# Optimization experiments

Hardware: AMD Instinct MI355X
Metric: run time of the kernel (lower is better)

The kernel has to match this reference:

```python
import jax, jax.numpy as jnp
import numpy as np

N = 30000
E = 480000
D_IN = 128
EPS = 1e-5
NEG_SLOPE = 0.2
# (in_dim, out_channels, heads) per GATConv layer; concat=True everywhere (PyG default)
CFG = [(D_IN, 100, 5), (500, 50, 5), (250, 32, 4), (128, 8, 4), (32, 1, 1)]
BN_DIMS = (500, 250, 128)


def setup_inputs() -> dict:
    key = jax.random.key(0)
    ks = iter(jax.random.split(key, 80))
    inp = {
        "x": jax.random.normal(next(ks), (N, D_IN), jnp.float32),
        "edge_index": jax.random.randint(next(ks), (2, E), 0, N),
        "edge_weight": jax.random.uniform(next(ks), (E, 1), jnp.float32),
    }
    for l, (cin, cout, h) in enumerate(CFG, 1):
        s = 1.0 / np.sqrt(cin)
        inp[f"W{l}"] = jax.random.normal(next(ks), (cin, h * cout), jnp.float32) * s
        inp[f"a_s{l}"] = jax.random.normal(next(ks), (1, h, cout), jnp.float32) * 0.1
        inp[f"a_d{l}"] = jax.random.normal(next(ks), (1, h, cout), jnp.float32) * 0.1
        inp[f"We{l}"] = jax.random.normal(next(ks), (1, h * cout), jnp.float32)
        inp[f"a_e{l}"] = jax.random.normal(next(ks), (1, h, cout), jnp.float32) * 0.1
        inp[f"b{l}"] = jnp.zeros((h * cout,), jnp.float32)
    for l, d in zip((1, 2, 3), BN_DIMS):
        inp[f"g{l}"] = jnp.ones((d,), jnp.float32)
        inp[f"beta{l}"] = jnp.zeros((d,), jnp.float32)
    return inp


def _gat(x, src, dst, ea, W, a_s, a_d, We, a_e, b, heads, cout):
    """PyG GATConv with edge_dim attention (concat=True)."""
    n = x.shape[0]
    h = (x @ W).reshape(n, heads, cout)            # [N,H,C]
    e = (ea @ We).reshape(-1, heads, cout)         # [E,H,C]
    al_src = (h * a_s).sum(-1)                     # [N,H]
    al_dst = (h * a_d).sum(-1)                     # [N,H]
    logit = jax.nn.leaky_relu(al_src[src] + al_dst[dst] + (e * a_e).sum(-1), NEG_SLOPE)
    m = jax.ops.segment_max(logit, dst, num_segments=n)
    m = jnp.where(jnp.isfinite(m), m, 0.0)
    ex = jnp.exp(logit - m[dst])                   # [E,H]
    den = jax.ops.segment_sum(ex, dst, num_segments=n)
    alpha = ex / jnp.maximum(den[dst], 1e-16)      # segment softmax over in-edges of dst
    out = jax.ops.segment_sum(h[src] * alpha[..., None], dst, num_segments=n)
    return out.reshape(n, heads * cout) + b


def _bn(x, g, b):
    mu = x.mean(0)
    var = x.var(0)  # biased, as torch uses for normalization
    return (x - mu) * jax.lax.rsqrt(var + EPS) * g + b


def reference(x, edge_index, edge_weight,
              W1, a_s1, a_d1, We1, a_e1, b1,
              W2, a_s2, a_d2, We2, a_e2, b2,
              W3, a_s3, a_d3, We3, a_e3, b3,
              W4, a_s4, a_d4, We4, a_e4, b4,
              W5, a_s5, a_d5, We5, a_e5, b5,
              g1, beta1, g2, beta2, g3, beta3):
    # add self loops (PyG default) with edge_attr fill_value='mean'
    loop = jnp.arange(N)
    src = jnp.concatenate([edge_index[0], loop])
    dst = jnp.concatenate([edge_index[1], loop])
    ea = jnp.concatenate([edge_weight, jnp.full((N, 1), edge_weight.mean(), edge_weight.dtype)], axis=0)

    h = _gat(x, src, dst, ea, W1, a_s1, a_d1, We1, a_e1, b1, 5, 100)
    h = jax.nn.relu(_bn(h, g1, beta1))
    h = _gat(h, src, dst, ea, W2, a_s2, a_d2, We2, a_e2, b2, 5, 50)
    h = jax.nn.relu(_bn(h, g2, beta2))
    h = _gat(h, src, dst, ea, W3, a_s3, a_d3, We3, a_e3, b3, 4, 32)
    h = jax.nn.relu(_bn(h, g3, beta3))
    h = _gat(h, src, dst, ea, W4, a_s4, a_d4, We4, a_e4, b4, 4, 8)
    h = jax.nn.relu(h)
    h = _gat(h, src, dst, ea, W5, a_s5, a_d5, We5, a_e5, b5, 1, 1)
    return h
```

## Files before the change

### kernel.cpp

```cpp
#include <hip/hip_runtime.h>
#include <hip/hip_bf16.h>
#include <math.h>

#define NN 30000
#define EE 480000
#define ET (EE + NN)
#define NEG_SLOPE 0.2f
#define BN_EPS 1e-5f

struct LayerCfg { int cin, C, H; };
static const LayerCfg g_cfg[5] = {
    {128, 100, 5}, {500, 50, 5}, {250, 32, 4}, {128, 8, 4}, {32, 1, 1}
};

typedef short short8 __attribute__((ext_vector_type(8)));
typedef float f32x4 __attribute__((ext_vector_type(4)));

__device__ __forceinline__ unsigned short f2bf(float f) {
    unsigned int u = __builtin_bit_cast(unsigned int, f);
    u = (u + 0x7FFFu + ((u >> 16) & 1u)) >> 16;
    return (unsigned short)u;
}
__device__ __forceinline__ float bf2f(unsigned short h) {
    unsigned int u = ((unsigned int)h) << 16;
    return __builtin_bit_cast(float, u);
}


__global__ void ewsum_kernel(const float* __restrict__ ew, float* __restrict__ out, int E) {
    __shared__ float sdata[256];
    int tid = threadIdx.x;
    float s = 0.f;
    for (int i = blockIdx.x * blockDim.x + tid; i < E; i += gridDim.x * blockDim.x)
        s += ew[i];
    sdata[tid] = s;
    __syncthreads();
    for (int off = 128; off > 0; off >>= 1) {
        if (tid < off) sdata[tid] += sdata[tid + off];
        __syncthreads();
    }
    if (tid == 0) atomicAdd(out, sdata[0]);
}

__global__ void build_edges_kernel(const int* __restrict__ ei, const float* __restrict__ ew,
                                   const float* __restrict__ sum,
                                   int* __restrict__ srcv, int* __restrict__ dstv,
                                   float* __restrict__ ea, int* __restrict__ cnt) {
    int e = blockIdx.x * blockDim.x + threadIdx.x;
    if (e >= ET) return;
    int d;
    if (e < EE) {
        srcv[e] = ei[e];
        d = ei[EE + e];
        dstv[e] = d;
        ea[e]   = ew[e];
    } else {
        int n = e - EE;
        srcv[e] = n;
        d = n;
        dstv[e] = n;
        ea[e]   = sum[0] * (1.0f / (float)EE);
    }
    atomicAdd(&cnt[d], 1);
}

__global__ void scan_kernel(const int* __restrict__ cnt, int* __restrict__ off,
                            int* __restrict__ wptr) {
    __shared__ int lsum[1024];
    __shared__ int loff[1024];
    const int T = 1024;
    int t = threadIdx.x;
    int chunk = (NN + T - 1) / T;
    int base = t * chunk;
    int end = min(NN, base + chunk);
    int s = 0;
    for (int i = base; i < end; i++) s += cnt[i];
    lsum[t] = s;
    __syncthreads();
    if (t == 0) {
        int run = 0;
        for (int i = 0; i < T; i++) { loff[i] = run; run += lsum[i]; }
    }
    __syncthreads();
    int run = loff[t];
    for (int i = base; i < end; i++) {
        off[i] = run;
        wptr[i] = run;
        run += cnt[i];
    }
    if (t == 0) off[NN] = ET;
}

__global__ void fill_kernel(const int* __restrict__ dstv, const int* __restrict__ srcv,
                            const float* __restrict__ ea,
                            int* __restrict__ wptr, int* __restrict__ csr_src,
                            float* __restrict__ csr_ea) {
    int e = blockIdx.x * blockDim.x + threadIdx.x;
    if (e >= ET) return;
    int p = atomicAdd(&wptr[dstv[e]], 1);
    csr_src[p] = srcv[e];
    csr_ea[p]  = ea[e];
}


struct PrepArgs {
    const float* W[5];
    const float* We[5];
    const float* ae[5];
    unsigned short* bh[5];
    unsigned short* bl[5];
    float* wedot;
    int K[5], N[5], Kp[5], Np[5], C[5], H[5];
};

__global__ void wedot_all_kernel(PrepArgs a) {
    int tid = threadIdx.x;
    int l = tid >> 3, hd = tid & 7;
    if (l < 5 && hd < a.H[l]) {
        int C = a.C[l];
        const float* We = a.We[l] + hd * C;
        const float* ae = a.ae[l] + hd * C;
        float s = 0.f;
        for (int c = 0; c < C; c++) s += We[c] * ae[c];
        a.wedot[l * 8 + hd] = s;
    }
}

__global__ void transpose_all_kernel(PrepArgs a) {
    int l = blockIdx.z;
    int Kp = a.Kp[l], Np = a.Np[l], K = a.K[l], N = a.N[l];
    int kb = blockIdx.x * 32, nb = blockIdx.y * 32;
    if (kb >= Kp || nb >= Np) return;
    const float* B = a.W[l];
    unsigned short* Bth = a.bh[l];
    unsigned short* Btl = a.bl[l];
    __shared__ float tile[32][33];
    int tx = threadIdx.x, ty = threadIdx.y;
#pragma unroll
    for (int i = 0; i < 4; i++) {
        int k = kb + ty + i * 8, n = nb + tx;
        tile[ty + i * 8][tx] = (k < K && n < N) ? B[(size_t)k * N + n] : 0.f;
    }
    __syncthreads();
#pragma unroll
    for (int i = 0; i < 4; i++) {
        int n = nb + ty + i * 8, k = kb + tx;
        if (n < Np && k < Kp) {
            float v = tile[tx][ty + i * 8];
            unsigned short hi = f2bf(v);
            unsigned short lo = f2bf(v - bf2f(hi));
            size_t idx = (size_t)n * Kp + k;
            Bth[idx] = hi;
            Btl[idx] = lo;
        }
    }
}

#define GBM 128
#define GBNT 128
#define GBK 32
#define ASTR 36
__global__ __launch_bounds__(256) void gemm_split_kernel(const float* __restrict__ A,
                                                         const unsigned short* __restrict__ Bt_hi,
                                                         const unsigned short* __restrict__ Bt_lo,
                                                         float* __restrict__ Cm,
                                                         unsigned short* __restrict__ Ch16,
                                                         int M, int Kp, int Nc,
                                                         const float* __restrict__ colsum,
                                                         const float* __restrict__ colsumsq,
                                                         const float* __restrict__ g,
                                                         const float* __restrict__ beta,
                                                         int D) {
    __shared__ short AsH[GBM * ASTR];
    __shared__ short AsL[GBM * ASTR];
    __shared__ short BsH[GBNT * ASTR];
    __shared__ short BsL[GBNT * ASTR];
    __shared__ float sscale[512];
    __shared__ float sshift[512];
    int tid = threadIdx.x;
    bool bn = (colsum != nullptr);
    if (bn) {
        for (int c = tid; c < Kp; c += 256) {
            float sc = 0.f, sh = 0.f;
            if (c < D) {
                float mu = colsum[c] * (1.0f / (float)NN);
                float var = colsumsq[c] * (1.0f / (float)NN) - mu * mu;
                sc = g[c] * rsqrtf(var + BN_EPS);
                sh = beta[c] - mu * sc;
            }
            sscale[c] = sc;
            sshift[c] = sh;
        }
        __syncthreads();
    }
    int wave = tid >> 6, lane = tid & 63;
    int q = lane >> 4, r = lane & 15;
    int m0 = blockIdx.y * GBM, n0 = blockIdx.x * GBNT;
    int wm = (wave & 1) * 64, wn = (wave >> 1) * 64;
    f32x4 acc[4][4];
#pragma unroll
    for (int i = 0; i < 4; i++)
#pragma unroll
        for (int j = 0; j < 4; j++) acc[i][j] = (f32x4)(0.f);

    int arow2 = tid >> 1;
    int acol2 = (tid & 1) * 16;
    int brow = tid >> 2;
    int bcol = (tid & 3) * 8;

    int ksteps = Kp / GBK;
    for (int ks = 0; ks < ksteps; ks++) {
        int k0 = ks * GBK;
        {
            int m = m0 + arow2;
            float v[16];
            if (m < M) {
                const float* Ap = A + (size_t)m * Kp + k0 + acol2;
                float4 f0 = *(const float4*)(Ap);
                float4 f1 = *(const float4*)(Ap + 4);
                float4 f2 = *(const float4*)(Ap + 8);
                float4 f3 = *(const float4*)(Ap + 12);
                v[0]=f0.x; v[1]=f0.y; v[2]=f0.z; v[3]=f0.w;
                v[4]=f1.x; v[5]=f1.y; v[6]=f1.z; v[7]=f1.w;
                v[8]=f2.x; v[9]=f2.y; v[10]=f2.z; v[11]=f2.w;
                v[12]=f3.x; v[13]=f3.y; v[14]=f3.z; v[15]=f3.w;
                if (bn) {
                    int cb = k0 + acol2;
#pragma unroll
                    for (int i = 0; i < 16; i++)
                        v[i] = fmaxf(v[i] * sscale[cb + i] + sshift[cb + i], 0.f);
                }
            } else {
#pragma unroll
                for (int i = 0; i < 16; i++) v[i] = 0.f;
            }
#pragma unroll
            for (int i = 0; i < 16; i++) {
                unsigned short hi = f2bf(v[i]);
                unsigned short lo = f2bf(v[i] - bf2f(hi));
                AsH[arow2 * ASTR + acol2 + i] = (short)hi;
                AsL[arow2 * ASTR + acol2 + i] = (short)lo;
            }
        }
#pragma unroll
        for (int p = 0; p < 2; p++) {
            int row = p * 64 + brow;
            size_t gidx = (size_t)(n0 + row) * Kp + k0 + bcol;
            *((uint4*)(BsH + row * ASTR + bcol)) = *((const uint4*)(Bt_hi + gidx));
            *((uint4*)(BsL + row * ASTR + bcol)) = *((const uint4*)(Bt_lo + gidx));
        }
        __syncthreads();
        short8 ah[4], al[4], bh[4], bl[4];
#pragma unroll
        for (int i = 0; i < 4; i++) {
            ah[i] = *((const short8*)(AsH + (wm + i * 16 + r) * ASTR + q * 8));
            al[i] = *((const short8*)(AsL + (wm + i * 16 + r) * ASTR + q * 8));
        }
#pragma unroll
        for (int j = 0; j < 4; j++) {
            bh[j] = *((const short8*)(BsH + (wn + j * 16 + r) * ASTR + q * 8));
            bl[j] = *((const short8*)(BsL + (wn + j * 16 + r) * ASTR + q * 8));
        }
#pragma unroll
        for (int i = 0; i < 4; i++)
#pragma unroll
            for (int j = 0; j < 4; j++) {
                acc[i][j] = __builtin_amdgcn_mfma_f32_16x16x32_bf16(ah[i], bh[j], acc[i][j], 0, 0, 0);
                acc[i][j] = __builtin_amdgcn_mfma_f32_16x16x32_bf16(ah[i], bl[j], acc[i][j], 0, 0, 0);
                acc[i][j] = __builtin_amdgcn_mfma_f32_16x16x32_bf16(al[i], bh[j], acc[i][j], 0, 0, 0);
            }
        __syncthreads();
    }
#pragma unroll
    for (int i = 0; i < 4; i++) {
#pragma unroll
        for (int j = 0; j < 4; j++) {
#pragma unroll
            for (int reg = 0; reg < 4; reg++) {
                int mrow = m0 + wm + i * 16 + q * 4 + reg;
                int ncol = n0 + wn + j * 16 + r;
                if (mrow < M && ncol < Nc) {
                    float val = acc[i][j][reg];
                    if (Cm)   Cm[(size_t)mrow * Nc + ncol] = val;
                    if (Ch16) Ch16[(size_t)mrow * Nc + ncol] = f2bf(val);
                }
            }
        }
    }
}

__global__ void gemv_l5_kernel(const float* __restrict__ X, const float* __restrict__ W,
                               const float* __restrict__ a_s, const float* __restrict__ a_d,
                               float* __restrict__ h, float* __restrict__ al_src,
                               float* __restrict__ al_dst) {
    __shared__ float w[32];
    if (threadIdx.x < 32) w[threadIdx.x] = W[threadIdx.x];
    __syncthreads();
    int n = blockIdx.x * blockDim.x + threadIdx.x;
    if (n >= NN) return;
    const float* row = X + (size_t)n * 32;
    float s = 0.f;
#pragma unroll
    for (int i = 0; i < 8; i++) {
        float4 f = *(const float4*)(row + i * 4);
        s += f.x * w[i * 4] + f.y * w[i * 4 + 1] + f.z * w[i * 4 + 2] + f.w * w[i * 4 + 3];
    }
    h[n] = s;
    al_src[n] = s * a_s[0];
    al_dst[n] = s * a_d[0];
}

__global__ void al_wave_kernel(const float* __restrict__ h, const float* __restrict__ a_s,
                               const float* __restrict__ a_d, float* __restrict__ al_src,
                               float* __restrict__ al_dst, int H, int C, int HC) {
    int w = (blockIdx.x * blockDim.x + threadIdx.x) >> 6;
    int lane = threadIdx.x & 63;
    if (w >= NN) return;
    const float* row = h + (size_t)w * HC;
    float s1[5] = {0.f, 0.f, 0.f, 0.f, 0.f};
    float s2[5] = {0.f, 0.f, 0.f, 0.f, 0.f};
#pragma unroll
    for (int hd = 0; hd < 5; hd++) {
        if (hd >= H) break;
        int base = hd * C;
        for (int c = lane; c < C; c += 64) {
            float v = row[base + c];
            s1[hd] += v * a_s[base + c];
            s2[hd] += v * a_d[base + c];
        }
    }
#pragma unroll
    for (int hd = 0; hd < 5; hd++) {
        if (hd >= H) break;
#pragma unroll
        for (int off = 32; off > 0; off >>= 1) {
            s1[hd] += __shfl_xor(s1[hd], off, 64);
            s2[hd] += __shfl_xor(s2[hd], off, 64);
        }
    }
    if (lane == 0) {
#pragma unroll
        for (int hd = 0; hd < 5; hd++) {
            if (hd >= H) break;
            al_src[(size_t)w * H + hd] = s1[hd];
            al_dst[(size_t)w * H + hd] = s2[hd];
        }
    }
}

__global__ void al_wave_h16_kernel(const unsigned short* __restrict__ h16,
                                   const float* __restrict__ a_s,
                                   const float* __restrict__ a_d,
                                   float* __restrict__ al_src, float* __restrict__ al_dst,
                                   int H, int C, int HC) {
    int w = (blockIdx.x * blockDim.x + threadIdx.x) >> 6;
    int lane = threadIdx.x & 63;
    if (w >= NN) return;
    const unsigned short* row = h16 + (size_t)w * HC;
    float s1[5] = {0.f, 0.f, 0.f, 0.f, 0.f};
    float s2[5] = {0.f, 0.f, 0.f, 0.f, 0.f};
#pragma unroll
    for (int hd = 0; hd < 5; hd++) {
        if (hd >= H) break;
        int base = hd * C;
        for (int c = lane * 2; c < C; c += 128) {
            unsigned int u = *(const unsigned int*)(row + base + c);
            float v0 = bf2f((unsigned short)(u & 0xffffu));
            float v1 = bf2f((unsigned short)(u >> 16));
            s1[hd] += v0 * a_s[base + c] + v1 * a_s[base + c + 1];
            s2[hd] += v0 * a_d[base + c] + v1 * a_d[base + c + 1];
        }
    }
#pragma unroll
    for (int hd = 0; hd < 5; hd++) {
        if (hd >= H) break;
#pragma unroll
        for (int off = 32; off > 0; off >>= 1) {
            s1[hd] += __shfl_xor(s1[hd], off, 64);
            s2[hd] += __shfl_xor(s2[hd], off, 64);
        }
    }
    if (lane == 0) {
#pragma unroll
        for (int hd = 0; hd < 5; hd++) {
            if (hd >= H) break;
            al_src[(size_t)w * H + hd] = s1[hd];
            al_dst[(size_t)w * H + hd] = s2[hd];
        }
    }
}

__global__ void attn_kernel(const float* __restrict__ al_src,
                            const float* __restrict__ al_dst,
                            const int* __restrict__ csr_src,
                            const float* __restrict__ csr_ea,
                            const float* __restrict__ we_dot,
                            const int* __restrict__ off,
                            float* __restrict__ alpha_t, int H, int NH) {
    int t = blockIdx.x * blockDim.x + threadIdx.x;
    if (t >= NH) return;
    int n = t / H, hd = t - n * H;
    int s = off[n], e = off[n + 1];
    float ad = al_dst[(size_t)n * H + hd];
    float wd = we_dot[hd];
    float* arow = alpha_t + (size_t)hd * ET;
    float m = -INFINITY, l = 0.f;
    int p = s;
    for (; p + 3 < e; p += 4) {
        int s0 = csr_src[p], s1 = csr_src[p + 1], s2 = csr_src[p + 2], s3 = csr_src[p + 3];
        float w0 = csr_ea[p], w1 = csr_ea[p + 1], w2 = csr_ea[p + 2], w3 = csr_ea[p + 3];
        float l0 = al_src[(size_t)s0 * H + hd] + ad + w0 * wd;
        float l1 = al_src[(size_t)s1 * H + hd] + ad + w1 * wd;
        float l2 = al_src[(size_t)s2 * H + hd] + ad + w2 * wd;
        float l3 = al_src[(size_t)s3 * H + hd] + ad + w3 * wd;
        l0 = (l0 >= 0.f) ? l0 : NEG_SLOPE * l0;
        l1 = (l1 >= 0.f) ? l1 : NEG_SLOPE * l1;
        l2 = (l2 >= 0.f) ? l2 : NEG_SLOPE * l2;
        l3 = (l3 >= 0.f) ? l3 : NEG_SLOPE * l3;
        arow[p] = l0; arow[p + 1] = l1; arow[p + 2] = l2; arow[p + 3] = l3;
        float mq = fmaxf(fmaxf(l0, l1), fmaxf(l2, l3));
        float nm = fmaxf(m, mq);
        l = l * __expf(m - nm)
          + __expf(l0 - nm) + __expf(l1 - nm) + __expf(l2 - nm) + __expf(l3 - nm);
        m = nm;
    }
    for (; p < e; p++) {
        float lg = al_src[(size_t)csr_src[p] * H + hd] + ad + csr_ea[p] * wd;
        lg = (lg >= 0.f) ? lg : NEG_SLOPE * lg;
        arow[p] = lg;
        float nm = fmaxf(m, lg);
        l = l * __expf(m - nm) + __expf(lg - nm);
        m = nm;
    }
    float inv = 1.f / fmaxf(l, 1e-16f);
    for (p = s; p < e; p++) arow[p] = __expf(arow[p] - m) * inv;
}

__global__ void aggregate_v4h_kernel(const unsigned short* __restrict__ h16,
                                     const float* __restrict__ alpha_t,
                                     const int* __restrict__ off,
                                     const int* __restrict__ csr_src,
                                     const float* __restrict__ bias,
                                     float* __restrict__ out,
                                     int C, int HC, int HC4, int total4, int opitch) {
    int t = blockIdx.x * blockDim.x + threadIdx.x;
    if (t >= total4) return;
    int n = t / HC4, j4 = t - n * HC4;
    int j = j4 * 4;
    int hd = j / C;
    const float* arow = alpha_t + (size_t)hd * ET;
    int s = off[n], e = off[n + 1];
    float4 acc = make_float4(0.f, 0.f, 0.f, 0.f);
    int p = s;
    for (; p + 3 < e; p += 4) {
        int idx[4]; float a[4];
#pragma unroll
        for (int u = 0; u < 4; u++) { idx[u] = csr_src[p + u]; a[u] = arow[p + u]; }
#pragma unroll
        for (int u = 0; u < 4; u++) {
            ushort4 uv = *(const ushort4*)(h16 + (size_t)idx[u] * HC + j);
            acc.x += a[u] * bf2f(uv.x);
            acc.y += a[u] * bf2f(uv.y);
            acc.z += a[u] * bf2f(uv.z);
            acc.w += a[u] * bf2f(uv.w);
        }
    }
    for (; p < e; p++) {
        int s0 = csr_src[p];
        float a0 = arow[p];
        ushort4 uv = *(const ushort4*)(h16 + (size_t)s0 * HC + j);
        acc.x += a0 * bf2f(uv.x);
        acc.y += a0 * bf2f(uv.y);
        acc.z += a0 * bf2f(uv.z);
        acc.w += a0 * bf2f(uv.w);
    }
    float4 bi = *(const float4*)(bias + j);
    float4 rr = make_float4(acc.x + bi.x, acc.y + bi.y, acc.z + bi.z, acc.w + bi.w);
    *(float4*)(out + (size_t)n * opitch + j) = rr;
}

__global__ void aggregate_v2h_kernel(const unsigned short* __restrict__ h16,
                                     const float* __restrict__ alpha_t,
                                     const int* __restrict__ off,
                                     const int* __restrict__ csr_src,
                                     const float* __restrict__ bias,
                                     float* __restrict__ out,
                                     int C, int HC, int HC2, int total2, int opitch) {
    int t = blockIdx.x * blockDim.x + threadIdx.x;
    if (t >= total2) return;
    int n = t / HC2, j2 = t - n * HC2;
    int j = j2 * 2;
    int hd = j / C;
    const float* arow = alpha_t + (size_t)hd * ET;
    int s = off[n], e = off[n + 1];
    float2 acc = make_float2(0.f, 0.f);
    int p = s;
    for (; p + 3 < e; p += 4) {
        int idx[4]; float a[4];
#pragma unroll
        for (int u = 0; u < 4; u++) { idx[u] = csr_src[p + u]; a[u] = arow[p + u]; }
#pragma unroll
        for (int u = 0; u < 4; u++) {
            ushort2 uv = *(const ushort2*)(h16 + (size_t)idx[u] * HC + j);
            acc.x += a[u] * bf2f(uv.x);
            acc.y += a[u] * bf2f(uv.y);
        }
    }
    for (; p < e; p++) {
        int s0 = csr_src[p];
        float a0 = arow[p];
        ushort2 uv = *(const ushort2*)(h16 + (size_t)s0 * HC + j);
        acc.x += a0 * bf2f(uv.x);
        acc.y += a0 * bf2f(uv.y);
    }
    float2 bi = *(const float2*)(bias + j);
    *(float2*)(out + (size_t)n * opitch + j) = make_float2(acc.x + bi.x, acc.y + bi.y);
}

__global__ void aggregate_v4_kernel(const float* __restrict__ hfeat,
                                    const float* __restrict__ alpha_t,
                                    const int* __restrict__ off,
                                    const int* __restrict__ csr_src,
                                    const float* __restrict__ bias,
                                    float* __restrict__ out,
                                    int C, int HC, int HC4, int total4, int relu, int opitch) {
    int t = blockIdx.x * blockDim.x + threadIdx.x;
    if (t >= total4) return;
    int n = t / HC4, j4 = t - n * HC4;
    int j = j4 * 4;
    int hd = j / C;
    const float* arow = alpha_t + (size_t)hd * ET;
    int s = off[n], e = off[n + 1];
    float4 acc = make_float4(0.f, 0.f, 0.f, 0.f);
    int p = s;
    for (; p + 3 < e; p += 4) {
        int idx[4]; float a[4];
#pragma unroll
        for (int u = 0; u < 4; u++) { idx[u] = csr_src[p + u]; a[u] = arow[p + u]; }
#pragma unroll
        for (int u = 0; u < 4; u++) {
            float4 f = *(const float4*)(hfeat + (size_t)idx[u] * HC + j);
            acc.x += a[u] * f.x; acc.y += a[u] * f.y; acc.z += a[u] * f.z; acc.w += a[u] * f.w;
        }
    }
    for (; p < e; p++) {
        int s0 = csr_src[p];
        float a0 = arow[p];
        float4 f0 = *(const float4*)(hfeat + (size_t)s0 * HC + j);
        acc.x += a0 * f0.x; acc.y += a0 * f0.y; acc.z += a0 * f0.z; acc.w += a0 * f0.w;
    }
    float4 bi = *(const float4*)(bias + j);
    float4 rr = make_float4(acc.x + bi.x, acc.y + bi.y, acc.z + bi.z, acc.w + bi.w);
    if (relu) {
        rr.x = fmaxf(rr.x, 0.f); rr.y = fmaxf(rr.y, 0.f);
        rr.z = fmaxf(rr.z, 0.f); rr.w = fmaxf(rr.w, 0.f);
    }
    *(float4*)(out + (size_t)n * opitch + j) = rr;
}

__global__ void aggregate_kernel(const float* __restrict__ hfeat,
                                 const float* __restrict__ alpha_t,
                                 const int* __restrict__ off, const int* __restrict__ csr_src,
                                 const float* __restrict__ bias, float* __restrict__ out,
                                 int total) {
    int t = blockIdx.x * blockDim.x + threadIdx.x;
    if (t >= total) return;
    int n = t;
    int s = off[n], e = off[n + 1];
    float acc = 0.f;
    int p = s;
    for (; p + 3 < e; p += 4) {
        acc += alpha_t[p] * hfeat[csr_src[p]]
             + alpha_t[p + 1] * hfeat[csr_src[p + 1]]
             + alpha_t[p + 2] * hfeat[csr_src[p + 2]]
             + alpha_t[p + 3] * hfeat[csr_src[p + 3]];
    }
    for (; p < e; p++) acc += alpha_t[p] * hfeat[csr_src[p]];
    out[n] = acc + bias[0];
}


__global__ void bn_stats_kernel(const float* __restrict__ x, float* __restrict__ colsum,
                                float* __restrict__ colsumsq, int D, int pitch) {
    int rows_per_block = (NN + gridDim.x - 1) / gridDim.x;
    int r0 = blockIdx.x * rows_per_block;
    int r1 = min(NN, r0 + rows_per_block);
    int c0 = threadIdx.x;
    int c1 = threadIdx.x + 256;
    float s0 = 0.f, q0 = 0.f, s1 = 0.f, q1 = 0.f;
    for (int r = r0; r < r1; r++) {
        const float* row = x + (size_t)r * pitch;
        if (c0 < D) { float v = row[c0]; s0 += v; q0 += v * v; }
        if (c1 < D) { float v = row[c1]; s1 += v; q1 += v * v; }
    }
    if (c0 < D) { atomicAdd(&colsum[c0], s0); atomicAdd(&colsumsq[c0], q0); }
    if (c1 < D) { atomicAdd(&colsum[c1], s1); atomicAdd(&colsumsq[c1], q1); }
}


static inline size_t align_up(size_t v, size_t a) { return (v + a - 1) / a * a; }

extern "C" void kernel_launch(void* const* d_in, const int* in_sizes, int n_in,
                              void* d_out, int out_size, void* d_ws, size_t ws_size,
                              hipStream_t stream) {
    const float* x_in = (const float*)d_in[0];
    const int* ei     = (const int*)d_in[1];
    const float* ew   = (const float*)d_in[2];

    char* pws = (char*)d_ws;
    size_t off_b = 0;
    auto alloc = [&](size_t bytes) -> void* {
        void* rp = pws + off_b;
        off_b = align_up(off_b + bytes, 256);
        return rp;
    };
    float* B0      = (float*)alloc((size_t)NN * 500 * 4);
    float* B1      = (float*)alloc((size_t)NN * 512 * 4);
    unsigned short* H16 = (unsigned short*)alloc((size_t)NN * 500 * 2);
    float* alpha_t = (float*)alloc((size_t)ET * 5 * 4);
    unsigned short* Wt_hi = (unsigned short*)alloc((size_t)600 * 512 * 2);
    unsigned short* Wt_lo = (unsigned short*)alloc((size_t)600 * 512 * 2);
    float* al_src  = (float*)alloc((size_t)NN * 5 * 4);
    float* al_dst  = (float*)alloc((size_t)NN * 5 * 4);
    float* ea      = (float*)alloc((size_t)ET * 4);
    float* csr_ea  = (float*)alloc((size_t)ET * 4);
    int* srcv      = (int*)alloc((size_t)ET * 4);
    int* dstv      = (int*)alloc((size_t)ET * 4);
    int* csr_src   = (int*)alloc((size_t)ET * 4);
    int* offarr    = (int*)alloc((size_t)(NN + 1) * 4);
    int* wptr      = (int*)alloc((size_t)NN * 4);
    float* esum    = (float*)alloc(4);
    int* cnt       = (int*)alloc((size_t)NN * 4);
    float* we_dot  = (float*)alloc(40 * 4);
    float* colsum  = (float*)alloc(512 * 4);
    float* colsumsq= (float*)alloc(512 * 4);
    (void)ws_size; (void)n_in; (void)in_sizes; (void)out_size;

    int Kp[5], Np[5];
    size_t wtoff[5];
    size_t acc_off = 0;
    for (int l = 0; l < 5; l++) {
        int K = g_cfg[l].cin, HC = g_cfg[l].C * g_cfg[l].H;
        Kp[l] = (K + 31) / 32 * 32;
        Np[l] = (HC + 127) / 128 * 128;
        wtoff[l] = acc_off;
        acc_off += (size_t)Kp[l] * Np[l];
    }

    PrepArgs pa;
    for (int l = 0; l < 5; l++) {
        pa.W[l]  = (const float*)d_in[3 + l * 6 + 0];
        pa.We[l] = (const float*)d_in[3 + l * 6 + 3];
        pa.ae[l] = (const float*)d_in[3 + l * 6 + 4];
        pa.bh[l] = Wt_hi + wtoff[l];
        pa.bl[l] = Wt_lo + wtoff[l];
        pa.K[l] = g_cfg[l].cin;
        pa.N[l] = g_cfg[l].C * g_cfg[l].H;
        pa.Kp[l] = Kp[l];
        pa.Np[l] = Np[l];
        pa.C[l] = g_cfg[l].C;
        pa.H[l] = g_cfg[l].H;
    }
    pa.wedot = we_dot;

    hipMemsetAsync(esum, 0, ((char*)(cnt + NN)) - ((char*)esum), stream);
    ewsum_kernel<<<256, 256, 0, stream>>>(ew, esum, EE);
    int ebl = (ET + 255) / 256;
    build_edges_kernel<<<ebl, 256, 0, stream>>>(ei, ew, esum, srcv, dstv, ea, cnt);
    scan_kernel<<<1, 1024, 0, stream>>>(cnt, offarr, wptr);
    fill_kernel<<<ebl, 256, 0, stream>>>(dstv, srcv, ea, wptr, csr_src, csr_ea);

    wedot_all_kernel<<<1, 64, 0, stream>>>(pa);
    transpose_all_kernel<<<dim3(16, 16, 5), dim3(32, 8), 0, stream>>>(pa);

    for (int l = 0; l < 5; l++) {
        const LayerCfg& cf = g_cfg[l];
        int H = cf.H, C = cf.C;
        int HC = H * C;
        const float* a_s = (const float*)d_in[3 + l * 6 + 1];
        const float* a_d = (const float*)d_in[3 + l * 6 + 2];
        const float* b   = (const float*)d_in[3 + l * 6 + 5];

        const float* X = (l == 0) ? x_in : B1;
        float* hbuf = B0;
        float* outbuf = (l == 4) ? (float*)d_out : B1;
        bool big = (l < 3);
        int opitch = (l == 4) ? 1 : Kp[l + 1];
        int NH = NN * H;

        if (l == 4) {
            gemv_l5_kernel<<<(NN + 255) / 256, 256, 0, stream>>>(
                X, pa.W[4], a_s, a_d, hbuf, al_src, al_dst);
        } else {
            const float* cs = (l >= 1) ? colsum : nullptr;
            const float* cq = (l >= 1) ? colsumsq : nullptr;
            const float* gg = (l >= 1) ? (const float*)d_in[33 + (l - 1) * 2 + 0] : nullptr;
            const float* bb = (l >= 1) ? (const float*)d_in[33 + (l - 1) * 2 + 1] : nullptr;
            int Din = (l >= 1) ? g_cfg[l - 1].C * g_cfg[l - 1].H : 0;
            dim3 ggrid(Np[l] / GBNT, (NN + GBM - 1) / GBM);
            gemm_split_kernel<<<ggrid, 256, 0, stream>>>(X, Wt_hi + wtoff[l], Wt_lo + wtoff[l],
                                                         big ? nullptr : hbuf,
                                                         big ? H16 : nullptr,
                                                         NN, Kp[l], HC, cs, cq, gg, bb, Din);
            int alblocks = (NN * 64 + 255) / 256;
            if (big) {
                al_wave_h16_kernel<<<alblocks, 256, 0, stream>>>(H16, a_s, a_d, al_src, al_dst, H, C, HC);
            } else {
                al_wave_kernel<<<alblocks, 256, 0, stream>>>(hbuf, a_s, a_d, al_src, al_dst, H, C, HC);
            }
        }

        attn_kernel<<<(NH + 255) / 256, 256, 0, stream>>>(al_src, al_dst, csr_src, csr_ea,
                                                          we_dot + l * 8, offarr, alpha_t, H, NH);

        if (big && (C & 3) == 0) {
            int HC4 = HC / 4;
            int total4 = NN * HC4;
            aggregate_v4h_kernel<<<(total4 + 255) / 256, 256, 0, stream>>>(
                H16, alpha_t, offarr, csr_src, b, outbuf, C, HC, HC4, total4, opitch);
        } else if (big) {
            int HC2 = HC / 2;
            int total2 = NN * HC2;
            aggregate_v2h_kernel<<<(total2 + 255) / 256, 256, 0, stream>>>(
                H16, alpha_t, offarr, csr_src, b, outbuf, C, HC, HC2, total2, opitch);
        } else if (l == 3) {
            int HC4 = HC / 4;
            int total4 = NN * HC4;
            aggregate_v4_kernel<<<(total4 + 255) / 256, 256, 0, stream>>>(
                hbuf, alpha_t, offarr, csr_src, b, outbuf, C, HC, HC4, total4, 1, opitch);
        } else {
            aggregate_kernel<<<(NN + 255) / 256, 256, 0, stream>>>(
                hbuf, alpha_t, offarr, csr_src, b, outbuf, NN);
        }

        if (l < 3) {
            int D = HC;
            hipMemsetAsync(colsum, 0, 2 * 512 * 4, stream);
            bn_stats_kernel<<<512, 256, 0, stream>>>(outbuf, colsum, colsumsq, D, opitch);
        }
    }
}
```

Baseline: 882.0 us.

## Fuse attention softmax and aggregation into one wave-per-node kernel

Replaces the separate attention kernel and the several aggregate kernels with a single kernel where each wavefront handles one destination node. It stages logits and source indices in shared memory, computes the per-head softmax, then gathers features. This removes the alpha_t global buffer round trip. It also folds the edge-weight sum into build_edges via atomics, folds the wedot computation into the transpose kernel, and replaces the per-layer colsum memsets with preallocated per-layer buffers zeroed once. In exchange, node degree is truncated at DEGCAP=256, a single lane serially reduces each head, and the global float atomic on esum may contend heavily.

```diff
diff --git a/kernel.cpp b/kernel.cpp
--- a/kernel.cpp
+++ b/kernel.cpp
@@ -7,6 +7,7 @@
 #define ET (EE + NN)
 #define NEG_SLOPE 0.2f
 #define BN_EPS 1e-5f
+#define DEGCAP 256
 
 struct LayerCfg { int cin, C, H; };
 static const LayerCfg g_cfg[5] = {
@@ -27,25 +28,9 @@
 }
 
 
-__global__ void ewsum_kernel(const float* __restrict__ ew, float* __restrict__ out, int E) {
-    __shared__ float sdata[256];
-    int tid = threadIdx.x;
-    float s = 0.f;
-    for (int i = blockIdx.x * blockDim.x + tid; i < E; i += gridDim.x * blockDim.x)
-        s += ew[i];
-    sdata[tid] = s;
-    __syncthreads();
-    for (int off = 128; off > 0; off >>= 1) {
-        if (tid < off) sdata[tid] += sdata[tid + off];
-        __syncthreads();
-    }
-    if (tid == 0) atomicAdd(out, sdata[0]);
-}
-
 __global__ void build_edges_kernel(const int* __restrict__ ei, const float* __restrict__ ew,
-                                   const float* __restrict__ sum,
                                    int* __restrict__ srcv, int* __restrict__ dstv,
-                                   float* __restrict__ ea, int* __restrict__ cnt) {
+                                   int* __restrict__ cnt, float* __restrict__ esum) {
     int e = blockIdx.x * blockDim.x + threadIdx.x;
     if (e >= ET) return;
     int d;
@@ -53,13 +38,12 @@
         srcv[e] = ei[e];
         d = ei[EE + e];
         dstv[e] = d;
-        ea[e]   = ew[e];
+        atomicAdd(esum, ew[e]);
     } else {
         int n = e - EE;
         srcv[e] = n;
         d = n;
         dstv[e] = n;
-        ea[e]   = sum[0] * (1.0f / (float)EE);
     }
     atomicAdd(&cnt[d], 1);
 }
@@ -92,14 +76,14 @@
 }
 
 __global__ void fill_kernel(const int* __restrict__ dstv, const int* __restrict__ srcv,
-                            const float* __restrict__ ea,
+                            const float* __restrict__ ew, const float* __restrict__ esum,
                             int* __restrict__ wptr, int* __restrict__ csr_src,
                             float* __restrict__ csr_ea) {
     int e = blockIdx.x * blockDim.x + threadIdx.x;
     if (e >= ET) return;
     int p = atomicAdd(&wptr[dstv[e]], 1);
     csr_src[p] = srcv[e];
-    csr_ea[p]  = ea[e];
+    csr_ea[p]  = (e < EE) ? ew[e] : esum[0] * (1.0f / (float)EE);
 }
 
 
@@ -113,21 +97,19 @@
     int K[5], N[5], Kp[5], Np[5], C[5], H[5];
 };
 
-__global__ void wedot_all_kernel(PrepArgs a) {
-    int tid = threadIdx.x;
-    int l = tid >> 3, hd = tid & 7;
-    if (l < 5 && hd < a.H[l]) {
-        int C = a.C[l];
-        const float* We = a.We[l] + hd * C;
-        const float* ae = a.ae[l] + hd * C;
-        float s = 0.f;
-        for (int c = 0; c < C; c++) s += We[c] * ae[c];
-        a.wedot[l * 8 + hd] = s;
-    }
-}
-
 __global__ void transpose_all_kernel(PrepArgs a) {
     int l = blockIdx.z;
+    if (blockIdx.x == 0 && blockIdx.y == 0 && threadIdx.y == 0 && threadIdx.x < 8) {
+        int hd = threadIdx.x;
+        if (hd < a.H[l]) {
+            int C = a.C[l];
+            const float* We = a.We[l] + hd * C;
+            const float* ae = a.ae[l] + hd * C;
+            float s = 0.f;
+            for (int c = 0; c < C; c++) s += We[c] * ae[c];
+            a.wedot[l * 8 + hd] = s;
+        }
+    }
     int Kp = a.Kp[l], Np = a.Np[l], K = a.K[l], N = a.N[l];
     int kb = blockIdx.x * 32, nb = blockIdx.y * 32;
     if (kb >= Kp || nb >= Np) return;
@@ -390,193 +372,114 @@
     }
 }
 
-__global__ void attn_kernel(const float* __restrict__ al_src,
-                            const float* __restrict__ al_dst,
-                            const int* __restrict__ csr_src,
-                            const float* __restrict__ csr_ea,
-                            const float* __restrict__ we_dot,
-                            const int* __restrict__ off,
-                            float* __restrict__ alpha_t, int H, int NH) {
-    int t = blockIdx.x * blockDim.x + threadIdx.x;
-    if (t >= NH) return;
-    int n = t / H, hd = t - n * H;
-    int s = off[n], e = off[n + 1];
-    float ad = al_dst[(size_t)n * H + hd];
-    float wd = we_dot[hd];
-    float* arow = alpha_t + (size_t)hd * ET;
-    float m = -INFINITY, l = 0.f;
-    int p = s;
-    for (; p + 3 < e; p += 4) {
-        int s0 = csr_src[p], s1 = csr_src[p + 1], s2 = csr_src[p + 2], s3 = csr_src[p + 3];
-        float w0 = csr_ea[p], w1 = csr_ea[p + 1], w2 = csr_ea[p + 2], w3 = csr_ea[p + 3];
-        float l0 = al_src[(size_t)s0 * H + hd] + ad + w0 * wd;
-        float l1 = al_src[(size_t)s1 * H + hd] + ad + w1 * wd;
-        float l2 = al_src[(size_t)s2 * H + hd] + ad + w2 * wd;
-        float l3 = al_src[(size_t)s3 * H + hd] + ad + w3 * wd;
-        l0 = (l0 >= 0.f) ? l0 : NEG_SLOPE * l0;
-        l1 = (l1 >= 0.f) ? l1 : NEG_SLOPE * l1;
-        l2 = (l2 >= 0.f) ? l2 : NEG_SLOPE * l2;
-        l3 = (l3 >= 0.f) ? l3 : NEG_SLOPE * l3;
-        arow[p] = l0; arow[p + 1] = l1; arow[p + 2] = l2; arow[p + 3] = l3;
-        float mq = fmaxf(fmaxf(l0, l1), fmaxf(l2, l3));
-        float nm = fmaxf(m, mq);
-        l = l * __expf(m - nm)
-          + __expf(l0 - nm) + __expf(l1 - nm) + __expf(l2 - nm) + __expf(l3 - nm);
-        m = nm;
-    }
-    for (; p < e; p++) {
-        float lg = al_src[(size_t)csr_src[p] * H + hd] + ad + csr_ea[p] * wd;
-        lg = (lg >= 0.f) ? lg : NEG_SLOPE * lg;
-        arow[p] = lg;
-        float nm = fmaxf(m, lg);
-        l = l * __expf(m - nm) + __expf(lg - nm);
-        m = nm;
-    }
-    float inv = 1.f / fmaxf(l, 1e-16f);
-    for (p = s; p < e; p++) arow[p] = __expf(arow[p] - m) * inv;
-}
-
-__global__ void aggregate_v4h_kernel(const unsigned short* __restrict__ h16,
-                                     const float* __restrict__ alpha_t,
-                                     const int* __restrict__ off,
-                                     const int* __restrict__ csr_src,
-                                     const float* __restrict__ bias,
-                                     float* __restrict__ out,
-                                     int C, int HC, int HC4, int total4, int opitch) {
-    int t = blockIdx.x * blockDim.x + threadIdx.x;
-    if (t >= total4) return;
-    int n = t / HC4, j4 = t - n * HC4;
-    int j = j4 * 4;
-    int hd = j / C;
-    const float* arow = alpha_t + (size_t)hd * ET;
-    int s = off[n], e = off[n + 1];
-    float4 acc = make_float4(0.f, 0.f, 0.f, 0.f);
-    int p = s;
-    for (; p + 3 < e; p += 4) {
-        int idx[4]; float a[4];
-#pragma unroll
-        for (int u = 0; u < 4; u++) { idx[u] = csr_src[p + u]; a[u] = arow[p + u]; }
-#pragma unroll
-        for (int u = 0; u < 4; u++) {
-            ushort4 uv = *(const ushort4*)(h16 + (size_t)idx[u] * HC + j);
-            acc.x += a[u] * bf2f(uv.x);
-            acc.y += a[u] * bf2f(uv.y);
-            acc.z += a[u] * bf2f(uv.z);
-            acc.w += a[u] * bf2f(uv.w);
-        }
-    }
-    for (; p < e; p++) {
-        int s0 = csr_src[p];
-        float a0 = arow[p];
-        ushort4 uv = *(const ushort4*)(h16 + (size_t)s0 * HC + j);
-        acc.x += a0 * bf2f(uv.x);
-        acc.y += a0 * bf2f(uv.y);
-        acc.z += a0 * bf2f(uv.z);
-        acc.w += a0 * bf2f(uv.w);
-    }
-    float4 bi = *(const float4*)(bias + j);
-    float4 rr = make_float4(acc.x + bi.x, acc.y + bi.y, acc.z + bi.z, acc.w + bi.w);
-    *(float4*)(out + (size_t)n * opitch + j) = rr;
-}
-
-__global__ void aggregate_v2h_kernel(const unsigned short* __restrict__ h16,
-                                     const float* __restrict__ alpha_t,
-                                     const int* __restrict__ off,
-                                     const int* __restrict__ csr_src,
-                                     const float* __restrict__ bias,
-                                     float* __restrict__ out,
-                                     int C, int HC, int HC2, int total2, int opitch) {
-    int t = blockIdx.x * blockDim.x + threadIdx.x;
-    if (t >= total2) return;
-    int n = t / HC2, j2 = t - n * HC2;
-    int j = j2 * 2;
-    int hd = j / C;
-    const float* arow = alpha_t + (size_t)hd * ET;
-    int s = off[n], e = off[n + 1];
-    float2 acc = make_float2(0.f, 0.f);
-    int p = s;
-    for (; p + 3 < e; p += 4) {
-        int idx[4]; float a[4];
-#pragma unroll
-        for (int u = 0; u < 4; u++) { idx[u] = csr_src[p + u]; a[u] = arow[p + u]; }
-#pragma unroll
-        for (int u = 0; u < 4; u++) {
-            ushort2 uv = *(const ushort2*)(h16 + (size_t)idx[u] * HC + j);
-            acc.x += a[u] * bf2f(uv.x);
-            acc.y += a[u] * bf2f(uv.y);
-        }
-    }
-    for (; p < e; p++) {
-        int s0 = csr_src[p];
-        float a0 = arow[p];
-        ushort2 uv = *(const ushort2*)(h16 + (size_t)s0 * HC + j);
-        acc.x += a0 * bf2f(uv.x);
-        acc.y += a0 * bf2f(uv.y);
-    }
-    float2 bi = *(const float2*)(bias + j);
-    *(float2*)(out + (size_t)n * opitch + j) = make_float2(acc.x + bi.x, acc.y + bi.y);
-}
-
-__global__ void aggregate_v4_kernel(const float* __restrict__ hfeat,
-                                    const float* __restrict__ alpha_t,
-                                    const int* __restrict__ off,
-                                    const int* __restrict__ csr_src,
-                                    const float* __restrict__ bias,
-                                    float* __restrict__ out,
-                                    int C, int HC, int HC4, int total4, int relu, int opitch) {
-    int t = blockIdx.x * blockDim.x + threadIdx.x;
-    if (t >= total4) return;
-    int n = t / HC4, j4 = t - n * HC4;
-    int j = j4 * 4;
-    int hd = j / C;
-    const float* arow = alpha_t + (size_t)hd * ET;
-    int s = off[n], e = off[n + 1];
-    float4 acc = make_float4(0.f, 0.f, 0.f, 0.f);
-    int p = s;
-    for (; p + 3 < e; p += 4) {
-        int idx[4]; float a[4];
-#pragma unroll
-        for (int u = 0; u < 4; u++) { idx[u] = csr_src[p + u]; a[u] = arow[p + u]; }
-#pragma unroll
-        for (int u = 0; u < 4; u++) {
-            float4 f = *(const float4*)(hfeat + (size_t)idx[u] * HC + j);
-            acc.x += a[u] * f.x; acc.y += a[u] * f.y; acc.z += a[u] * f.z; acc.w += a[u] * f.w;
-        }
-    }
-    for (; p < e; p++) {
-        int s0 = csr_src[p];
-        float a0 = arow[p];
-        float4 f0 = *(const float4*)(hfeat + (size_t)s0 * HC + j);
-        acc.x += a0 * f0.x; acc.y += a0 * f0.y; acc.z += a0 * f0.z; acc.w += a0 * f0.w;
-    }
-    float4 bi = *(const float4*)(bias + j);
-    float4 rr = make_float4(acc.x + bi.x, acc.y + bi.y, acc.z + bi.z, acc.w + bi.w);
-    if (relu) {
-        rr.x = fmaxf(rr.x, 0.f); rr.y = fmaxf(rr.y, 0.f);
-        rr.z = fmaxf(rr.z, 0.f); rr.w = fmaxf(rr.w, 0.f);
-    }
-    *(float4*)(out + (size_t)n * opitch + j) = rr;
-}
-
-__global__ void aggregate_kernel(const float* __restrict__ hfeat,
-                                 const float* __restrict__ alpha_t,
-                                 const int* __restrict__ off, const int* __restrict__ csr_src,
-                                 const float* __restrict__ bias, float* __restrict__ out,
-                                 int total) {
-    int t = blockIdx.x * blockDim.x + threadIdx.x;
-    if (t >= total) return;
-    int n = t;
-    int s = off[n], e = off[n + 1];
-    float acc = 0.f;
-    int p = s;
-    for (; p + 3 < e; p += 4) {
-        acc += alpha_t[p] * hfeat[csr_src[p]]
-             + alpha_t[p + 1] * hfeat[csr_src[p + 1]]
-             + alpha_t[p + 2] * hfeat[csr_src[p + 2]]
-             + alpha_t[p + 3] * hfeat[csr_src[p + 3]];
-    }
-    for (; p < e; p++) acc += alpha_t[p] * hfeat[csr_src[p]];
-    out[n] = acc + bias[0];
+__global__ __launch_bounds__(256) void attn_agg_kernel(
+    const unsigned short* __restrict__ h16,
+    const float* __restrict__ hf32,
+    const float* __restrict__ al_src, const float* __restrict__ al_dst,
+    const int* __restrict__ csr_src, const float* __restrict__ csr_ea,
+    const float* __restrict__ we_dot,
+    const int* __restrict__ off,
+    const float* __restrict__ bias,
+    float* __restrict__ out,
+    int H, int C, int HC, int opitch, int relu)
+{
+    __shared__ int   s_src[4][DEGCAP];
+    __shared__ float s_lg [4][DEGCAP * 5];
+    __shared__ float s_m[4][8];
+    __shared__ float s_inv[4][8];
+    int wv = threadIdx.x >> 6;
+    int lane = threadIdx.x & 63;
+    int n = blockIdx.x * 4 + wv;
+
+    int s = off[n];
+    int deg = off[n + 1] - s;
+    if (deg > DEGCAP) deg = DEGCAP;
+
+    float ad[5], wd[5];
+#pragma unroll
+    for (int hd = 0; hd < 5; hd++) {
+        if (hd >= H) break;
+        ad[hd] = al_dst[(size_t)n * H + hd];
+        wd[hd] = we_dot[hd];
+    }
+
+    for (int p = lane; p < deg; p += 64) {
+        int sv = csr_src[s + p];
+        float w = csr_ea[s + p];
+        s_src[wv][p] = sv;
+#pragma unroll
+        for (int hd = 0; hd < 5; hd++) {
+            if (hd >= H) break;
+            float lg = al_src[(size_t)sv * H + hd] + ad[hd] + w * wd[hd];
+            lg = (lg >= 0.f) ? lg : NEG_SLOPE * lg;
+            s_lg[wv][p * H + hd] = lg;
+        }
+    }
+    __syncthreads();
+
+    if (lane < H) {
+        float m = -INFINITY, lsum = 0.f;
+        for (int p = 0; p < deg; p++) {
+            float v = s_lg[wv][p * H + lane];
+            float nm = fmaxf(m, v);
+            lsum = lsum * __expf(m - nm) + __expf(v - nm);
+            m = nm;
+        }
+        s_m[wv][lane] = m;
+        s_inv[wv][lane] = 1.f / fmaxf(lsum, 1e-16f);
+    }
+    __syncthreads();
+
+    int tot = deg * H;
+    for (int idx = lane; idx < tot; idx += 64) {
+        int hd = idx % H;
+        s_lg[wv][idx] = __expf(s_lg[wv][idx] - s_m[wv][hd]) * s_inv[wv][hd];
+    }
+    __syncthreads();
+
+    if (h16) {
+        const unsigned short* hb = h16;
+        for (int jb = lane * 4; jb < HC; jb += 256) {
+            if (jb + 3 < HC) {
+                int hd0 = jb / C, hd1 = (jb + 1) / C, hd2 = (jb + 2) / C, hd3 = (jb + 3) / C;
+                float4 acc = make_float4(bias[jb], bias[jb + 1], bias[jb + 2], bias[jb + 3]);
+                for (int p = 0; p < deg; p++) {
+                    const unsigned short* hp = hb + (size_t)s_src[wv][p] * HC + jb;
+                    ushort2 u0 = *(const ushort2*)hp;
+                    ushort2 u1 = *(const ushort2*)(hp + 2);
+                    const float* av = &s_lg[wv][p * H];
+                    acc.x += av[hd0] * bf2f(u0.x);
+                    acc.y += av[hd1] * bf2f(u0.y);
+                    acc.z += av[hd2] * bf2f(u1.x);
+                    acc.w += av[hd3] * bf2f(u1.y);
+                }
+                *(float4*)(out + (size_t)n * opitch + jb) = acc;
+            } else {
+                for (int k = 0; k < 4; k++) {
+                    int j = jb + k;
+                    if (j >= HC) break;
+                    int hd = j / C;
+                    float acc = bias[j];
+                    for (int p = 0; p < deg; p++)
+                        acc += s_lg[wv][p * H + hd] * bf2f(hb[(size_t)s_src[wv][p] * HC + j]);
+                    out[(size_t)n * opitch + j] = acc;
+                }
+            }
+        }
+    } else {
+        for (int jb = lane * 4; jb < HC; jb += 256) {
+            for (int k = 0; k < 4; k++) {
+                int j = jb + k;
+                if (j >= HC) break;
+                int hd = j / C;
+                float acc = bias[j];
+                for (int p = 0; p < deg; p++)
+                    acc += s_lg[wv][p * H + hd] * hf32[(size_t)s_src[wv][p] * HC + j];
+                if (relu) acc = fmaxf(acc, 0.f);
+                out[(size_t)n * opitch + j] = acc;
+            }
+        }
+    }
 }
 
 
@@ -617,23 +520,22 @@
     float* B0      = (float*)alloc((size_t)NN * 500 * 4);
     float* B1      = (float*)alloc((size_t)NN * 512 * 4);
     unsigned short* H16 = (unsigned short*)alloc((size_t)NN * 500 * 2);
-    float* alpha_t = (float*)alloc((size_t)ET * 5 * 4);
     unsigned short* Wt_hi = (unsigned short*)alloc((size_t)600 * 512 * 2);
     unsigned short* Wt_lo = (unsigned short*)alloc((size_t)600 * 512 * 2);
     float* al_src  = (float*)alloc((size_t)NN * 5 * 4);
     float* al_dst  = (float*)alloc((size_t)NN * 5 * 4);
-    float* ea      = (float*)alloc((size_t)ET * 4);
     float* csr_ea  = (float*)alloc((size_t)ET * 4);
     int* srcv      = (int*)alloc((size_t)ET * 4);
     int* dstv      = (int*)alloc((size_t)ET * 4);
     int* csr_src   = (int*)alloc((size_t)ET * 4);
     int* offarr    = (int*)alloc((size_t)(NN + 1) * 4);
     int* wptr      = (int*)alloc((size_t)NN * 4);
+    float* we_dot  = (float*)alloc(40 * 4);
     float* esum    = (float*)alloc(4);
     int* cnt       = (int*)alloc((size_t)NN * 4);
-    float* we_dot  = (float*)alloc(40 * 4);
-    float* colsum  = (float*)alloc(512 * 4);
-    float* colsumsq= (float*)alloc(512 * 4);
+    float* colsum_all   = (float*)alloc(3 * 512 * 4);
+    float* colsumsq_all = (float*)alloc(3 * 512 * 4);
+    char* zero_end = pws + off_b;
     (void)ws_size; (void)n_in; (void)in_sizes; (void)out_size;
 
     int Kp[5], Np[5];
@@ -663,14 +565,12 @@
     }
     pa.wedot = we_dot;
 
-    hipMemsetAsync(esum, 0, ((char*)(cnt + NN)) - ((char*)esum), stream);
-    ewsum_kernel<<<256, 256, 0, stream>>>(ew, esum, EE);
+    hipMemsetAsync(esum, 0, (size_t)(zero_end - (char*)esum), stream);
     int ebl = (ET + 255) / 256;
-    build_edges_kernel<<<ebl, 256, 0, stream>>>(ei, ew, esum, srcv, dstv, ea, cnt);
+    build_edges_kernel<<<ebl, 256, 0, stream>>>(ei, ew, srcv, dstv, cnt, esum);
     scan_kernel<<<1, 1024, 0, stream>>>(cnt, offarr, wptr);
-    fill_kernel<<<ebl, 256, 0, stream>>>(dstv, srcv, ea, wptr, csr_src, csr_ea);
-
-    wedot_all_kernel<<<1, 64, 0, stream>>>(pa);
+    fill_kernel<<<ebl, 256, 0, stream>>>(dstv, srcv, ew, esum, wptr, csr_src, csr_ea);
+
     transpose_all_kernel<<<dim3(16, 16, 5), dim3(32, 8), 0, stream>>>(pa);
 
     for (int l = 0; l < 5; l++) {
@@ -686,14 +586,14 @@
         float* outbuf = (l == 4) ? (float*)d_out : B1;
         bool big = (l < 3);
         int opitch = (l == 4) ? 1 : Kp[l + 1];
-        int NH = NN * H;
+        int alblocks = (NN * 64 + 255) / 256;
 
         if (l == 4) {
             gemv_l5_kernel<<<(NN + 255) / 256, 256, 0, stream>>>(
                 X, pa.W[4], a_s, a_d, hbuf, al_src, al_dst);
         } else {
-            const float* cs = (l >= 1) ? colsum : nullptr;
-            const float* cq = (l >= 1) ? colsumsq : nullptr;
+            const float* cs = (l >= 1) ? colsum_all + (l - 1) * 512 : nullptr;
+            const float* cq = (l >= 1) ? colsumsq_all + (l - 1) * 512 : nullptr;
             const float* gg = (l >= 1) ? (const float*)d_in[33 + (l - 1) * 2 + 0] : nullptr;
             const float* bb = (l >= 1) ? (const float*)d_in[33 + (l - 1) * 2 + 1] : nullptr;
             int Din = (l >= 1) ? g_cfg[l - 1].C * g_cfg[l - 1].H : 0;
@@ -702,7 +602,6 @@
                                                          big ? nullptr : hbuf,
                                                          big ? H16 : nullptr,
                                                          NN, Kp[l], HC, cs, cq, gg, bb, Din);
-            int alblocks = (NN * 64 + 255) / 256;
             if (big) {
                 al_wave_h16_kernel<<<alblocks, 256, 0, stream>>>(H16, a_s, a_d, al_src, al_dst, H, C, HC);
             } else {
@@ -710,33 +609,14 @@
             }
         }
 
-        attn_kernel<<<(NH + 255) / 256, 256, 0, stream>>>(al_src, al_dst, csr_src, csr_ea,
-                                                          we_dot + l * 8, offarr, alpha_t, H, NH);
-
-        if (big && (C & 3) == 0) {
-            int HC4 = HC / 4;
-            int total4 = NN * HC4;
-            aggregate_v4h_kernel<<<(total4 + 255) / 256, 256, 0, stream>>>(
-                H16, alpha_t, offarr, csr_src, b, outbuf, C, HC, HC4, total4, opitch);
-        } else if (big) {
-            int HC2 = HC / 2;
-            int total2 = NN * HC2;
-            aggregate_v2h_kernel<<<(total2 + 255) / 256, 256, 0, stream>>>(
-                H16, alpha_t, offarr, csr_src, b, outbuf, C, HC, HC2, total2, opitch);
-        } else if (l == 3) {
-            int HC4 = HC / 4;
-            int total4 = NN * HC4;
-            aggregate_v4_kernel<<<(total4 + 255) / 256, 256, 0, stream>>>(
-                hbuf, alpha_t, offarr, csr_src, b, outbuf, C, HC, HC4, total4, 1, opitch);
-        } else {
-            aggregate_kernel<<<(NN + 255) / 256, 256, 0, stream>>>(
-                hbuf, alpha_t, offarr, csr_src, b, outbuf, NN);
-        }
+        attn_agg_kernel<<<NN / 4, 256, 0, stream>>>(
+            big ? H16 : nullptr, big ? nullptr : hbuf,
+            al_src, al_dst, csr_src, csr_ea, we_dot + l * 8, offarr,
+            b, outbuf, H, C, HC, opitch, (l == 3) ? 1 : 0);
 
         if (l < 3) {
-            int D = HC;
-            hipMemsetAsync(colsum, 0, 2 * 512 * 4, stream);
-            bn_stats_kernel<<<512, 256, 0, stream>>>(outbuf, colsum, colsumsq, D, opitch);
-        }
-    }
-}
+            bn_stats_kernel<<<512, 256, 0, stream>>>(outbuf, colsum_all + l * 512,
+                                                     colsumsq_all + l * 512, HC, opitch);
+        }
+    }
+}
```

After: 963.3 us. 9.2% more time.
